# Kernel tuning notes

Hardware: AMD Instinct MI355X
Metric: run time of the kernel (lower is better)

## Reference

```python
import jax, jax.numpy as jnp
import numpy as np

B, S, D = 2, 4096, 2048
EXPAND, K = 2, 4
DI = EXPAND * D
EPS = 1e-5


def setup_inputs() -> dict:
    key = jax.random.key(0)
    ks = jax.random.split(key, 7)
    scale = lambda d: 1.0 / np.sqrt(d)
    return {
        "x": jax.random.normal(ks[0], (B, S, D), dtype=jnp.float32),
        "w_norm": jnp.ones((D,), dtype=jnp.float32),
        "W_up": jax.random.normal(ks[1], (D, DI), dtype=jnp.float32) * scale(D),
        "W_gate": jax.random.normal(ks[2], (D, DI), dtype=jnp.float32) * scale(D),
        "W_down": jax.random.normal(ks[3], (DI, D), dtype=jnp.float32) * scale(DI),
        "conv_w": jax.random.normal(ks[4], (DI, 1, K), dtype=jnp.float32) * scale(K),
        "conv_b": jnp.zeros((DI,), dtype=jnp.float32),
    }


def _rmsnorm(x, w, eps=EPS):
    ms = jnp.mean(jnp.square(x.astype(jnp.float32)), axis=-1, keepdims=True)
    return x * jax.lax.rsqrt(ms + eps).astype(x.dtype) * w


def _causal_dwconv(h, conv_w, conv_b):
    # h: [B, S, DI] -> depthwise causal conv along S
    hc = jnp.transpose(h, (0, 2, 1))  # [B, DI, S]
    y = jax.lax.conv_general_dilated(
        hc, conv_w, window_strides=(1,), padding=[(K - 1, 0)],
        feature_group_count=DI, dimension_numbers=("NCH", "OIH", "NCH"))
    y = y + conv_b[None, :, None]
    return jnp.transpose(y, (0, 2, 1))  # [B, S, DI]


def reference(x, w_norm, W_up, W_gate, W_down, conv_w, conv_b):
    normed = _rmsnorm(x, w_norm)                       # [B,S,D]
    val = _causal_dwconv(normed @ W_up, conv_w, conv_b)  # [B,S,DI]
    gated = jax.nn.silu(normed @ W_gate) * val          # [B,S,DI]
    return x + gated @ W_down                           # [B,S,D]
```

## Files before the change

kernel.cpp:

```cpp
#include <hip/hip_runtime.h>
#include <stdint.h>

#define B_   2
#define S_   4096
#define D_   2048
#define DI_  4096
#define M_   (B_ * S_)
#define EPS_ 1e-5f
#define SCH_ 8

typedef __bf16 bf16x8 __attribute__((ext_vector_type(8)));
typedef float  f32x4  __attribute__((ext_vector_type(4)));
typedef uint16_t u16x8 __attribute__((ext_vector_type(8)));

__device__ __forceinline__ uint16_t f32_to_bf16(float f) {
    uint32_t u = __builtin_bit_cast(uint32_t, f);
    uint32_t r = (u + 0x7fffu + ((u >> 16) & 1u)) >> 16;
    return (uint16_t)r;
}
__device__ __forceinline__ float bf16_to_f32(uint16_t h) {
    return __builtin_bit_cast(float, (uint32_t)h << 16);
}

typedef const __attribute__((address_space(1))) uint32_t* gptr_t;
typedef __attribute__((address_space(3))) uint32_t* lptr_t;

__device__ __forceinline__ void gll16(const void* g, void* l) {
    __builtin_amdgcn_global_load_lds((gptr_t)g, (lptr_t)l, 16, 0, 0);
}

__global__ __launch_bounds__(256)
void transpose_bf16_kernel(const float* __restrict__ W, uint16_t* __restrict__ WT,
                           int K, int N) {
    __shared__ float tile[32][33];
    const int nb = N / 32;
    const int tn = blockIdx.x % nb;
    const int tk = blockIdx.x / nb;
    const int tx = threadIdx.x & 31;
    const int ty = threadIdx.x >> 5;
    const int gk = tk * 32, gn = tn * 32;
#pragma unroll
    for (int i = 0; i < 4; i++) {
        int k = ty + i * 8;
        tile[k][tx] = W[(size_t)(gk + k) * N + gn + tx];
    }
    __syncthreads();
#pragma unroll
    for (int i = 0; i < 4; i++) {
        int n = ty + i * 8;
        WT[(size_t)(gn + n) * K + gk + tx] = f32_to_bf16(tile[tx][n]);
    }
}

__global__ __launch_bounds__(256)
void rmsnorm_kernel(const float* __restrict__ x, const float* __restrict__ w,
                    uint16_t* __restrict__ out) {
    const int row  = blockIdx.x;
    const int tid  = threadIdx.x;
    const int lane = tid & 63, wid = tid >> 6;
    const float* xr = x + (size_t)row * D_;

    f32x4 a = *(const f32x4*)&xr[tid * 8];
    f32x4 b = *(const f32x4*)&xr[tid * 8 + 4];
    float ss = a[0]*a[0] + a[1]*a[1] + a[2]*a[2] + a[3]*a[3]
             + b[0]*b[0] + b[1]*b[1] + b[2]*b[2] + b[3]*b[3];
#pragma unroll
    for (int off = 32; off > 0; off >>= 1) ss += __shfl_xor(ss, off);

    __shared__ float red[4];
    if (lane == 0) red[wid] = ss;
    __syncthreads();
    const float tot = red[0] + red[1] + red[2] + red[3];
    const float scale = rsqrtf(tot * (1.0f / D_) + EPS_);

    f32x4 wa = *(const f32x4*)&w[tid * 8];
    f32x4 wb = *(const f32x4*)&w[tid * 8 + 4];
    u16x8 o;
#pragma unroll
    for (int j = 0; j < 4; j++) o[j]     = f32_to_bf16(a[j] * scale * wa[j]);
#pragma unroll
    for (int j = 0; j < 4; j++) o[j + 4] = f32_to_bf16(b[j] * scale * wb[j]);
    *(u16x8*)&out[(size_t)row * D_ + tid * 8] = o;
}

template <int EPI>
__global__ __launch_bounds__(512, 2)
void gemm8p_kernel(const uint16_t* __restrict__ A, const uint16_t* __restrict__ BT,
                   int M, int N, int K,
                   float* __restrict__ Cf, uint16_t* __restrict__ Cb,
                   uint16_t* __restrict__ Cb2, const float* __restrict__ resid) {
    __shared__ uint16_t As[2][16384];
    __shared__ uint16_t Bs[2][16384];

    const int nwg = gridDim.x;
    const int cpx = nwg >> 3;
    const int bid = blockIdx.x;
    const int swz = (bid & 7) * cpx + (bid >> 3);

    const int nbn  = N >> 8;
    const int bm   = swz / nbn;
    const int bn   = swz % nbn;
    const int brow = bm << 8, bcol = bn << 8;
    const int tid  = threadIdx.x;
    const int wid  = tid >> 6, lane = tid & 63;
    const int wr   = wid >> 2, wc = wid & 3;
    const int fr   = lane & 15;
    const int kx0 = (((lane >> 4) << 3)) ^ ((lane & 7) << 3);
    const int kx1 = kx0 ^ 32;
    int rhoN[4];
#pragma unroll
    for (int n = 0; n < 4; n++) rhoN[n] = ((n >> 1) << 7) + (wc << 5) + ((n & 1) << 4) + fr;

    const uint16_t* ApS[4];
    const uint16_t* BpS[4];
#pragma unroll
    for (int i = 0; i < 4; i++) {
        const int z  = (i << 13) + (wid << 10) + (lane << 4);
        const int zz = z ^ (((z >> 7) & 7) << 4);
        const int row = zz >> 7;
        const int kk  = (zz >> 1) & 63;
        ApS[i] = A + (size_t)(brow + row) * K + kk;
        const int h = row >> 7, q = (row >> 5) & 3, j = row & 31;
        BpS[i] = BT + (size_t)(bcol + q * 64 + h * 32 + j) * K + kk;
    }

    f32x4 acc[8][4];
#pragma unroll
    for (int i = 0; i < 8; i++)
#pragma unroll
        for (int j = 0; j < 4; j++) acc[i][j] = (f32x4){0.f, 0.f, 0.f, 0.f};

    const int nt = K >> 6;

#pragma unroll
    for (int i = 0; i < 4; i++) gll16(ApS[i], &As[0][i * 4096 + wid * 512]);
#pragma unroll
    for (int i = 0; i < 4; i++) gll16(BpS[i], &Bs[0][i * 4096 + wid * 512]);
    asm volatile("s_waitcnt vmcnt(0)" ::: "memory");
    __builtin_amdgcn_s_barrier();

    bf16x8 aF[8], bF[8];

    for (int t = 0; t < nt; ++t) {
        const int cur = t & 1, nxt = cur ^ 1;
        const int kn  = (t + 1) << 6;
        const bool pf = (t + 1) < nt;

#pragma unroll
        for (int mh = 0; mh < 4; ++mh) {
            const int r = (wr << 7) + (mh << 4) + fr;
            aF[mh * 2 + 0] = *(const bf16x8*)&As[cur][r * 64 + kx0];
            aF[mh * 2 + 1] = *(const bf16x8*)&As[cur][r * 64 + kx1];
        }
#pragma unroll
        for (int n = 0; n < 2; ++n) {
            bF[n * 2 + 0] = *(const bf16x8*)&Bs[cur][rhoN[n] * 64 + kx0];
            bF[n * 2 + 1] = *(const bf16x8*)&Bs[cur][rhoN[n] * 64 + kx1];
        }
        if (pf) {
            gll16(ApS[0] + kn, &As[nxt][0 * 4096 + wid * 512]);
            gll16(ApS[2] + kn, &As[nxt][2 * 4096 + wid * 512]);
        }
        __builtin_amdgcn_s_barrier();
        __builtin_amdgcn_s_setprio(1);
#pragma unroll
        for (int mh = 0; mh < 4; ++mh)
#pragma unroll
            for (int n = 0; n < 2; ++n)
#pragma unroll
                for (int ks = 0; ks < 2; ++ks)
                    acc[mh][n] = __builtin_amdgcn_mfma_f32_16x16x32_bf16(
                        aF[mh * 2 + ks], bF[n * 2 + ks], acc[mh][n], 0, 0, 0);
        __builtin_amdgcn_s_setprio(0);
        asm volatile("s_waitcnt vmcnt(4)" ::: "memory");
        __builtin_amdgcn_s_barrier();

#pragma unroll
        for (int n = 2; n < 4; ++n) {
            bF[n * 2 + 0] = *(const bf16x8*)&Bs[cur][rhoN[n] * 64 + kx0];
            bF[n * 2 + 1] = *(const bf16x8*)&Bs[cur][rhoN[n] * 64 + kx1];
        }
        if (pf) {
            gll16(BpS[0] + kn, &Bs[nxt][0 * 4096 + wid * 512]);
            gll16(BpS[1] + kn, &Bs[nxt][1 * 4096 + wid * 512]);
        }
        __builtin_amdgcn_s_barrier();
        __builtin_amdgcn_s_setprio(1);
#pragma unroll
        for (int mh = 0; mh < 4; ++mh)
#pragma unroll
            for (int n = 2; n < 4; ++n)
#pragma unroll
                for (int ks = 0; ks < 2; ++ks)
                    acc[mh][n] = __builtin_amdgcn_mfma_f32_16x16x32_bf16(
                        aF[mh * 2 + ks], bF[n * 2 + ks], acc[mh][n], 0, 0, 0);
        __builtin_amdgcn_s_setprio(0);
        asm volatile("s_waitcnt vmcnt(4)" ::: "memory");
        __builtin_amdgcn_s_barrier();

#pragma unroll
        for (int mh = 0; mh < 4; ++mh) {
            const int r = (wr << 7) + 64 + (mh << 4) + fr;
            aF[mh * 2 + 0] = *(const bf16x8*)&As[cur][r * 64 + kx0];
            aF[mh * 2 + 1] = *(const bf16x8*)&As[cur][r * 64 + kx1];
        }
        if (pf) {
            gll16(BpS[2] + kn, &Bs[nxt][2 * 4096 + wid * 512]);
            gll16(BpS[3] + kn, &Bs[nxt][3 * 4096 + wid * 512]);
        }
        __builtin_amdgcn_s_barrier();
        __builtin_amdgcn_s_setprio(1);
#pragma unroll
        for (int mh = 0; mh < 4; ++mh)
#pragma unroll
            for (int n = 2; n < 4; ++n)
#pragma unroll
                for (int ks = 0; ks < 2; ++ks)
                    acc[4 + mh][n] = __builtin_amdgcn_mfma_f32_16x16x32_bf16(
                        aF[mh * 2 + ks], bF[n * 2 + ks], acc[4 + mh][n], 0, 0, 0);
        __builtin_amdgcn_s_setprio(0);
        __builtin_amdgcn_s_barrier();

        if (pf) {
            gll16(ApS[1] + kn, &As[nxt][1 * 4096 + wid * 512]);
            gll16(ApS[3] + kn, &As[nxt][3 * 4096 + wid * 512]);
        }
        __builtin_amdgcn_s_barrier();
        __builtin_amdgcn_s_setprio(1);
#pragma unroll
        for (int mh = 0; mh < 4; ++mh)
#pragma unroll
            for (int n = 0; n < 2; ++n)
#pragma unroll
                for (int ks = 0; ks < 2; ++ks)
                    acc[4 + mh][n] = __builtin_amdgcn_mfma_f32_16x16x32_bf16(
                        aF[mh * 2 + ks], bF[n * 2 + ks], acc[4 + mh][n], 0, 0, 0);
        __builtin_amdgcn_s_setprio(0);
        asm volatile("s_waitcnt vmcnt(4)" ::: "memory");
        __builtin_amdgcn_s_barrier();
    }

    const int r0 = (lane >> 4) << 2;
    const bool upHalf = (bcol < DI_);
#pragma unroll
    for (int m = 0; m < 8; ++m) {
        const int row = brow + (wr << 7) + ((m >> 2) << 6) + ((m & 3) << 4) + r0;
#pragma unroll
        for (int n = 0; n < 4; ++n) {
            const int col = bcol + (wc << 6) + (n << 4) + fr;
#pragma unroll
            for (int r = 0; r < 4; ++r) {
                const float v = acc[m][n][r];
                if (EPI == 0) {
                    const size_t idx = (size_t)(row + r) * N + col;
                    Cf[idx] = v + resid[idx];
                } else {
                    if (upHalf) {
                        Cb[(size_t)(row + r) * DI_ + col] = f32_to_bf16(v);
                    } else {
                        const float s = v / (1.0f + __expf(-v));
                        Cb2[(size_t)(row + r) * DI_ + (col - DI_)] = f32_to_bf16(s);
                    }
                }
            }
        }
    }
}

__global__ __launch_bounds__(256)
void conv_mul_kernel(const uint16_t* __restrict__ up, uint16_t* __restrict__ sg,
                     const float* __restrict__ cw, const float* __restrict__ cb) {
    const size_t gid = (size_t)blockIdx.x * 256 + threadIdx.x;
    const int c8 = (int)(gid % (DI_ / 8));
    const int sc = (int)((gid / (DI_ / 8)) % (S_ / SCH_));
    const int b  = (int)(gid / ((size_t)(DI_ / 8) * (S_ / SCH_)));
    const int c0 = c8 * 8;
    const int s0 = sc * SCH_;

    f32x4 wv[8];
#pragma unroll
    for (int j = 0; j < 8; j++) wv[j] = *(const f32x4*)&cw[(c0 + j) * 4];
    const f32x4 b0 = *(const f32x4*)&cb[c0];
    const f32x4 b1 = *(const f32x4*)&cb[c0 + 4];

    const uint16_t* upb = up + (size_t)b * S_ * DI_ + c0;
    uint16_t*       sgb = sg + (size_t)b * S_ * DI_ + c0;

    u16x8 win[3];
#pragma unroll
    for (int i = 0; i < 3; i++) {
        const int ss = s0 - 3 + i;
        if (ss >= 0) {
            win[i] = *(const u16x8*)&upb[(size_t)ss * DI_];
        } else {
#pragma unroll
            for (int j = 0; j < 8; j++) win[i][j] = 0;
        }
    }

#pragma unroll
    for (int st = 0; st < SCH_; ++st) {
        const size_t roff = (size_t)(s0 + st) * DI_;
        const u16x8 curv = *(const u16x8*)&upb[roff];
        const u16x8 gv   = *(const u16x8*)&sgb[roff];
        u16x8 o;
#pragma unroll
        for (int j = 0; j < 8; j++) {
            const float bias = (j < 4) ? b0[j] : b1[j - 4];
            const float a = bias
                + bf16_to_f32(win[0][j]) * wv[j][0]
                + bf16_to_f32(win[1][j]) * wv[j][1]
                + bf16_to_f32(win[2][j]) * wv[j][2]
                + bf16_to_f32(curv[j])   * wv[j][3];
            o[j] = f32_to_bf16(bf16_to_f32(gv[j]) * a);
        }
        *(u16x8*)&sgb[roff] = o;
        win[0] = win[1]; win[1] = win[2]; win[2] = curv;
    }
}

extern "C" void kernel_launch(void* const* d_in, const int* in_sizes, int n_in,
                              void* d_out, int out_size, void* d_ws, size_t ws_size,
                              hipStream_t stream) {
    const float* x      = (const float*)d_in[0];
    const float* w_norm = (const float*)d_in[1];
    const float* W_up   = (const float*)d_in[2];
    const float* W_gate = (const float*)d_in[3];
    const float* W_down = (const float*)d_in[4];
    const float* conv_w = (const float*)d_in[5];
    const float* conv_b = (const float*)d_in[6];
    float* out = (float*)d_out;

    char* ws = (char*)d_ws;
    uint16_t* normed = (uint16_t*)ws;  ws += (size_t)M_  * D_  * 2;
    uint16_t* WupT   = (uint16_t*)ws;  ws += (size_t)DI_ * D_  * 2;
    uint16_t* WgateT = (uint16_t*)ws;  ws += (size_t)DI_ * D_  * 2;
    uint16_t* WdownT = (uint16_t*)ws;  ws += (size_t)D_  * DI_ * 2;
    uint16_t* up     = (uint16_t*)ws;  ws += (size_t)M_  * DI_ * 2;
    uint16_t* sg     = (uint16_t*)ws;  ws += (size_t)M_  * DI_ * 2;

    transpose_bf16_kernel<<<(D_ / 32) * (DI_ / 32), 256, 0, stream>>>(W_up,   WupT,   D_,  DI_);
    transpose_bf16_kernel<<<(D_ / 32) * (DI_ / 32), 256, 0, stream>>>(W_gate, WgateT, D_,  DI_);
    transpose_bf16_kernel<<<(DI_ / 32) * (D_ / 32), 256, 0, stream>>>(W_down, WdownT, DI_, D_);

    rmsnorm_kernel<<<M_, 256, 0, stream>>>(x, w_norm, normed);

    gemm8p_kernel<3><<<(M_ / 256) * ((2 * DI_) / 256), 512, 0, stream>>>(
        normed, WupT, M_, 2 * DI_, D_, nullptr, up, sg, nullptr);

    conv_mul_kernel<<<(int)(((size_t)B_ * (S_ / SCH_) * (DI_ / 8)) / 256), 256, 0, stream>>>(
        up, sg, conv_w, conv_b);

    gemm8p_kernel<0><<<(M_ / 256) * (D_ / 256), 512, 0, stream>>>(
        sg, WdownT, M_, D_, DI_, out, nullptr, nullptr, x);
}
```

Before: 502.0 us.

## Prefetch two K-tiles ahead and remap workgroups to XCD-grouped tiles

The GEMM main loop now issues global-to-LDS loads for tile t+2 into the buffer just consumed, replacing the previous one-tile-ahead prefetch. This gives each load more time to land before it is needed, with adjusted vmcnt waits. The block-to-tile mapping is also reworked so each XCD owns a contiguous band of N columns, grouped in row chunks, to improve L2 reuse. The cost is tighter reliance on exact waitcnt bookkeeping, since a buffer is overwritten while other waves may still be reading it, which risks races.

```diff
diff --git a/kernel.cpp b/kernel.cpp
--- a/kernel.cpp
+++ b/kernel.cpp
@@ -92,24 +92,27 @@
     __shared__ uint16_t As[2][16384];
     __shared__ uint16_t Bs[2][16384];
 
-    const int nwg = gridDim.x;
-    const int cpx = nwg >> 3;
+    const int nbn = N >> 8;
     const int bid = blockIdx.x;
-    const int swz = (bid & 7) * cpx + (bid >> 3);
-
-    const int nbn  = N >> 8;
-    const int bm   = swz / nbn;
-    const int bn   = swz % nbn;
+    const int xcd = bid & 7;
+    const int j   = bid >> 3;
+    const int wc_ = nbn >> 3;
+    const int wlog = 31 - __clz(wc_);
+    const int g   = j >> 5;
+    const int rr  = j & 31;
+    const int bm  = g * (32 >> wlog) + (rr >> wlog);
+    const int bn  = (xcd << wlog) + (rr & (wc_ - 1));
+
     const int brow = bm << 8, bcol = bn << 8;
     const int tid  = threadIdx.x;
     const int wid  = tid >> 6, lane = tid & 63;
-    const int wr   = wid >> 2, wc = wid & 3;
+    const int wr   = wid >> 2, wcv = wid & 3;
     const int fr   = lane & 15;
     const int kx0 = (((lane >> 4) << 3)) ^ ((lane & 7) << 3);
     const int kx1 = kx0 ^ 32;
     int rhoN[4];
 #pragma unroll
-    for (int n = 0; n < 4; n++) rhoN[n] = ((n >> 1) << 7) + (wc << 5) + ((n & 1) << 4) + fr;
+    for (int n = 0; n < 4; n++) rhoN[n] = ((n >> 1) << 7) + (wcv << 5) + ((n & 1) << 4) + fr;
 
     const uint16_t* ApS[4];
     const uint16_t* BpS[4];
@@ -120,31 +123,43 @@
         const int row = zz >> 7;
         const int kk  = (zz >> 1) & 63;
         ApS[i] = A + (size_t)(brow + row) * K + kk;
-        const int h = row >> 7, q = (row >> 5) & 3, j = row & 31;
-        BpS[i] = BT + (size_t)(bcol + q * 64 + h * 32 + j) * K + kk;
+        const int h = row >> 7, q = (row >> 5) & 3, jj = row & 31;
+        BpS[i] = BT + (size_t)(bcol + q * 64 + h * 32 + jj) * K + kk;
     }
 
     f32x4 acc[8][4];
 #pragma unroll
     for (int i = 0; i < 8; i++)
 #pragma unroll
-        for (int j = 0; j < 4; j++) acc[i][j] = (f32x4){0.f, 0.f, 0.f, 0.f};
+        for (int jn = 0; jn < 4; jn++) acc[i][jn] = (f32x4){0.f, 0.f, 0.f, 0.f};
 
     const int nt = K >> 6;
 
-#pragma unroll
-    for (int i = 0; i < 4; i++) gll16(ApS[i], &As[0][i * 4096 + wid * 512]);
-#pragma unroll
-    for (int i = 0; i < 4; i++) gll16(BpS[i], &Bs[0][i * 4096 + wid * 512]);
-    asm volatile("s_waitcnt vmcnt(0)" ::: "memory");
+    gll16(ApS[0], &As[0][0 * 4096 + wid * 512]);
+    gll16(ApS[2], &As[0][2 * 4096 + wid * 512]);
+    gll16(BpS[0], &Bs[0][0 * 4096 + wid * 512]);
+    gll16(BpS[1], &Bs[0][1 * 4096 + wid * 512]);
+    gll16(BpS[2], &Bs[0][2 * 4096 + wid * 512]);
+    gll16(BpS[3], &Bs[0][3 * 4096 + wid * 512]);
+    gll16(ApS[1], &As[0][1 * 4096 + wid * 512]);
+    gll16(ApS[3], &As[0][3 * 4096 + wid * 512]);
+    gll16(ApS[0] + 64, &As[1][0 * 4096 + wid * 512]);
+    gll16(ApS[2] + 64, &As[1][2 * 4096 + wid * 512]);
+    gll16(BpS[0] + 64, &Bs[1][0 * 4096 + wid * 512]);
+    gll16(BpS[1] + 64, &Bs[1][1 * 4096 + wid * 512]);
+    gll16(BpS[2] + 64, &Bs[1][2 * 4096 + wid * 512]);
+    gll16(BpS[3] + 64, &Bs[1][3 * 4096 + wid * 512]);
+    gll16(ApS[1] + 64, &As[1][1 * 4096 + wid * 512]);
+    gll16(ApS[3] + 64, &As[1][3 * 4096 + wid * 512]);
+    asm volatile("s_waitcnt vmcnt(8)" ::: "memory");
     __builtin_amdgcn_s_barrier();
 
     bf16x8 aF[8], bF[8];
 
     for (int t = 0; t < nt; ++t) {
-        const int cur = t & 1, nxt = cur ^ 1;
-        const int kn  = (t + 1) << 6;
-        const bool pf = (t + 1) < nt;
+        const int cur = t & 1;
+        const int kn2 = (t + 2) << 6;
+        const bool pf2 = (t + 2) < nt;
 
 #pragma unroll
         for (int mh = 0; mh < 4; ++mh) {
@@ -157,10 +172,6 @@
             bF[n * 2 + 0] = *(const bf16x8*)&Bs[cur][rhoN[n] * 64 + kx0];
             bF[n * 2 + 1] = *(const bf16x8*)&Bs[cur][rhoN[n] * 64 + kx1];
         }
-        if (pf) {
-            gll16(ApS[0] + kn, &As[nxt][0 * 4096 + wid * 512]);
-            gll16(ApS[2] + kn, &As[nxt][2 * 4096 + wid * 512]);
-        }
         __builtin_amdgcn_s_barrier();
         __builtin_amdgcn_s_setprio(1);
 #pragma unroll
@@ -172,7 +183,8 @@
                     acc[mh][n] = __builtin_amdgcn_mfma_f32_16x16x32_bf16(
                         aF[mh * 2 + ks], bF[n * 2 + ks], acc[mh][n], 0, 0, 0);
         __builtin_amdgcn_s_setprio(0);
-        asm volatile("s_waitcnt vmcnt(4)" ::: "memory");
+        if (t + 1 < nt) { asm volatile("s_waitcnt vmcnt(8)" ::: "memory"); }
+        else            { asm volatile("s_waitcnt vmcnt(0)" ::: "memory"); }
         __builtin_amdgcn_s_barrier();
 
 #pragma unroll
@@ -180,9 +192,11 @@
             bF[n * 2 + 0] = *(const bf16x8*)&Bs[cur][rhoN[n] * 64 + kx0];
             bF[n * 2 + 1] = *(const bf16x8*)&Bs[cur][rhoN[n] * 64 + kx1];
         }
-        if (pf) {
-            gll16(BpS[0] + kn, &Bs[nxt][0 * 4096 + wid * 512]);
-            gll16(BpS[1] + kn, &Bs[nxt][1 * 4096 + wid * 512]);
+        if (pf2) {
+            gll16(ApS[0] + kn2, &As[cur][0 * 4096 + wid * 512]);
+            gll16(ApS[2] + kn2, &As[cur][2 * 4096 + wid * 512]);
+            gll16(BpS[0] + kn2, &Bs[cur][0 * 4096 + wid * 512]);
+            gll16(BpS[1] + kn2, &Bs[cur][1 * 4096 + wid * 512]);
         }
         __builtin_amdgcn_s_barrier();
         __builtin_amdgcn_s_setprio(1);
@@ -195,7 +209,6 @@
                     acc[mh][n] = __builtin_amdgcn_mfma_f32_16x16x32_bf16(
                         aF[mh * 2 + ks], bF[n * 2 + ks], acc[mh][n], 0, 0, 0);
         __builtin_amdgcn_s_setprio(0);
-        asm volatile("s_waitcnt vmcnt(4)" ::: "memory");
         __builtin_amdgcn_s_barrier();
 
 #pragma unroll
@@ -204,10 +217,6 @@
             aF[mh * 2 + 0] = *(const bf16x8*)&As[cur][r * 64 + kx0];
             aF[mh * 2 + 1] = *(const bf16x8*)&As[cur][r * 64 + kx1];
         }
-        if (pf) {
-            gll16(BpS[2] + kn, &Bs[nxt][2 * 4096 + wid * 512]);
-            gll16(BpS[3] + kn, &Bs[nxt][3 * 4096 + wid * 512]);
-        }
         __builtin_amdgcn_s_barrier();
         __builtin_amdgcn_s_setprio(1);
 #pragma unroll
@@ -221,9 +230,11 @@
         __builtin_amdgcn_s_setprio(0);
         __builtin_amdgcn_s_barrier();
 
-        if (pf) {
-            gll16(ApS[1] + kn, &As[nxt][1 * 4096 + wid * 512]);
-            gll16(ApS[3] + kn, &As[nxt][3 * 4096 + wid * 512]);
+        if (pf2) {
+            gll16(BpS[2] + kn2, &Bs[cur][2 * 4096 + wid * 512]);
+            gll16(BpS[3] + kn2, &Bs[cur][3 * 4096 + wid * 512]);
+            gll16(ApS[1] + kn2, &As[cur][1 * 4096 + wid * 512]);
+            gll16(ApS[3] + kn2, &As[cur][3 * 4096 + wid * 512]);
         }
         __builtin_amdgcn_s_barrier();
         __builtin_amdgcn_s_setprio(1);
@@ -236,7 +247,8 @@
                     acc[4 + mh][n] = __builtin_amdgcn_mfma_f32_16x16x32_bf16(
                         aF[mh * 2 + ks], bF[n * 2 + ks], acc[4 + mh][n], 0, 0, 0);
         __builtin_amdgcn_s_setprio(0);
-        asm volatile("s_waitcnt vmcnt(4)" ::: "memory");
+        if (pf2) { asm volatile("s_waitcnt vmcnt(12)" ::: "memory"); }
+        else     { asm volatile("s_waitcnt vmcnt(4)" ::: "memory"); }
         __builtin_amdgcn_s_barrier();
     }
 
@@ -247,7 +259,7 @@
         const int row = brow + (wr << 7) + ((m >> 2) << 6) + ((m & 3) << 4) + r0;
 #pragma unroll
         for (int n = 0; n < 4; ++n) {
-            const int col = bcol + (wc << 6) + (n << 4) + fr;
+            const int col = bcol + (wcv << 6) + (n << 4) + fr;
 #pragma unroll
             for (int r = 0; r < 4; ++r) {
                 const float v = acc[m][n][r];
```

Measured after the change: 525.3 us. 4.6% more time.
